# Kernel tuning notes

Measured on AMD Instinct MI355X. Metric: run time of the kernel, lower is better.

The kernel has to match this reference:

```python
import jax, jax.numpy as jnp
import numpy as np

H, L, N = 512, 4096, 64

def make_dplr_hippo(n):
    # HiPPO-LegS -> NPLR -> DPLR diagonalization (numpy, init-time only)
    p0 = np.sqrt(1 + 2 * np.arange(n))
    A = p0[:, None] * p0[None, :]
    A = -(np.tril(A) - np.diag(np.arange(n)))
    p = np.sqrt(np.arange(n) + 0.5)
    b = np.sqrt(2 * np.arange(n) + 1.0)
    S = A + p[:, None] * p[None, :]
    Lambda_re = np.full(n, np.diagonal(S).mean())
    Lambda_im, V = np.linalg.eigh(S * -1j)
    Pc = V.conj().T @ p
    Bc = V.conj().T @ b
    return Lambda_re, Lambda_im, Pc, Bc

def setup_inputs() -> dict:
    key = jax.random.key(0)
    k_u, k_c, k_s = jax.random.split(key, 3)
    lr, li, Pc, Bc = make_dplr_hippo(N)
    tile = lambda v: jnp.tile(jnp.asarray(v, jnp.float32)[None, :], (H, 1))
    dt_min, dt_max = 0.001, 0.1
    log_step = (jax.random.uniform(k_s, (H, 1), jnp.float32)
                * (np.log(dt_max) - np.log(dt_min)) + np.log(dt_min))
    return {
        "u": jax.random.normal(k_u, (H, L), jnp.float32),
        "Lambda_re": tile(lr), "Lambda_im": tile(li),
        "P_re": tile(Pc.real), "P_im": tile(Pc.imag),
        "B_re": tile(Bc.real), "B_im": tile(Bc.imag),
        "C": jax.random.normal(k_c, (H, N, 2), jnp.float32) * (0.5 ** 0.5),
        "D": jnp.ones((H, 1), jnp.float32),
        "log_step": log_step,
    }

def reference(u, Lambda_re, Lambda_im, P_re, P_im, B_re, B_im, C, D, log_step):
    # u: [H, L]; all params leading dim H (vmapped channels)
    Lam = jnp.minimum(Lambda_re, -1e-4) + 1j * Lambda_im      # [H, N]
    P = P_re + 1j * P_im                                       # [H, N]
    B = B_re + 1j * B_im                                       # [H, N]
    Cc = C[..., 0] + 1j * C[..., 1]                             # [H, N]
    step = jnp.exp(log_step)                                    # [H, 1]
    Lseq = u.shape[-1]
    Omega = jnp.exp(-2j * jnp.pi * (jnp.arange(Lseq) / Lseq)).astype(jnp.complex64)  # [L]
    g = (2.0 / step) * ((1.0 - Omega) / (1.0 + Omega))[None, :]  # [H, L]
    c = 2.0 / (1.0 + Omega)                                      # [L]
    denom = 1.0 / (g[:, :, None] - Lam[:, None, :])              # [H, L, N]
    cauchy = lambda v: jnp.einsum('hn,hln->hl', v, denom)
    k00 = cauchy(Cc.conj() * B)
    k01 = cauchy(Cc.conj() * P)
    k10 = cauchy(P.conj() * B)
    k11 = cauchy(P.conj() * P)
    atRoots = c[None, :] * (k00 - k01 * (1.0 / (1.0 + k11)) * k10)
    K = jnp.fft.ifft(atRoots, Lseq, axis=-1).real                # [H, L] conv kernel
    # causal convolution via zero-padded FFT (length 2L)
    ud = jnp.fft.rfft(u, n=2 * Lseq, axis=-1)
    Kd = jnp.fft.rfft(K, n=2 * Lseq, axis=-1)
    y = jnp.fft.irfft(ud * Kd, n=2 * Lseq, axis=-1)[..., :Lseq]
    return y + D * u
```

## Files before the change

kernel.cpp:

```cpp
#include <hip/hip_runtime.h>
#include <math.h>

#define NT 512

typedef float v2 __attribute__((ext_vector_type(2)));

__device__ __forceinline__ v2 vrot(v2 a){ return (v2){-a.y, a.x}; }
__device__ __forceinline__ v2 vconj(v2 a){ return (v2){a.x, -a.y}; }

__device__ __forceinline__ v2 pk_addrot(v2 a, v2 b){
    v2 d;
    asm("v_pk_add_f32 %0, %1, %2 op_sel:[0,1] op_sel_hi:[1,0] neg_lo:[0,1] neg_hi:[0,0]"
        : "=v"(d) : "v"(a), "v"(b));
    return d;
}
__device__ __forceinline__ v2 pk_subrot(v2 a, v2 b){
    v2 d;
    asm("v_pk_add_f32 %0, %1, %2 op_sel:[0,1] op_sel_hi:[1,0] neg_lo:[0,0] neg_hi:[0,1]"
        : "=v"(d) : "v"(a), "v"(b));
    return d;
}
__device__ __forceinline__ v2 vcmul(v2 a, v2 b){
    v2 d;
    asm("v_pk_mul_f32 %0, %1, %2 op_sel:[0,0] op_sel_hi:[0,1]"
        : "=v"(d) : "v"(a), "v"(b));
    asm("v_pk_fma_f32 %0, %1, %2, %0 op_sel:[1,1,0] op_sel_hi:[1,0,1] neg_lo:[0,1,0] neg_hi:[0,0,0]"
        : "+v"(d) : "v"(a), "v"(b));
    return d;
}
__device__ __forceinline__ v2 vcmulc(v2 a, v2 b){
    v2 d;
    asm("v_pk_mul_f32 %0, %1, %2 op_sel:[0,0] op_sel_hi:[0,1] neg_lo:[0,0] neg_hi:[0,1]"
        : "=v"(d) : "v"(a), "v"(b));
    asm("v_pk_fma_f32 %0, %1, %2, %0 op_sel:[1,1,0] op_sel_hi:[1,0,1]"
        : "+v"(d) : "v"(a), "v"(b));
    return d;
}
__device__ __forceinline__ void cacc(v2& acc, v2 w, v2 p){
    asm("v_pk_fma_f32 %0, %1, %2, %0 op_sel:[0,0,0] op_sel_hi:[1,0,1]"
        : "+v"(acc) : "s"(w), "v"(p));
    asm("v_pk_fma_f32 %0, %1, %2, %0 op_sel:[1,1,0] op_sel_hi:[0,1,1] neg_hi:[0,1,0]"
        : "+v"(acc) : "s"(w), "v"(p));
}
__device__ __forceinline__ void racc(v2& acc, v2 wp, v2 p){
    asm("v_pk_fma_f32 %0, %1, %2, %0 op_sel:[0,0,0] op_sel_hi:[1,1,1] neg_hi:[0,1,0]"
        : "+v"(acc) : "s"(wp), "v"(p));
}

__device__ __forceinline__ int SW(int e){ return e ^ (((e>>5) ^ (e>>9)) & 15); }

__device__ __forceinline__ v2& q512(v2* buf, int tbs, int k){
    return *(v2*)((char*)buf + ((tbs ^ (k<<3)) + (k<<12)));
}
__device__ __forceinline__ v2& q512u(v2* buf, int tbs, int k){
    return *(v2*)((char*)buf + (((tbs ^ 64) ^ (k<<3)) + (k<<12) + 32768));
}

__device__ __forceinline__ int d8r4(int x){
    return ((x&7)<<9) | (((x>>3)&7)<<6) | (((x>>6)&7)<<3) | ((x>>9)&7);
}
__device__ __forceinline__ int rev3(int t){
    return ((t&7)<<6) | (t&56) | ((t>>6)&7);
}

__device__ __forceinline__ void load_row(const v2* twd, int rowIdx, v2 W[7]) {
    const float4* rp4 = (const float4*)(twd + rowIdx*8);
    float4 q0 = rp4[0], q1 = rp4[1], q2 = rp4[2], q3 = rp4[3];
    W[0]=(v2){q0.x,q0.y}; W[1]=(v2){q0.z,q0.w}; W[2]=(v2){q1.x,q1.y};
    W[3]=(v2){q1.z,q1.w}; W[4]=(v2){q2.x,q2.y}; W[5]=(v2){q2.z,q2.w};
    W[6]=(v2){q3.x,q3.y};
}

__device__ __forceinline__ void dft8_inv(v2 t[8], v2 y[8]) {
    const float RH = 0.70710678f;
    v2 p  = t[0]+t[4], m  = t[0]-t[4], q  = t[2]+t[6], r  = t[2]-t[6];
    v2 E0 = p+q, E2 = p-q;
    v2 E1 = pk_addrot(m, r), E3 = pk_subrot(m, r);
    v2 p2 = t[1]+t[5], m2 = t[1]-t[5], q2 = t[3]+t[7], r2 = t[3]-t[7];
    v2 O0 = p2+q2, O2 = p2-q2;
    v2 O1 = pk_addrot(m2, r2), O3 = pk_subrot(m2, r2);
    v2 W1O = RH * pk_addrot(O1, O1);
    v2 A3  = RH * pk_addrot(O3, O3);
    y[0] = E0 + O0;  y[4] = E0 - O0;
    y[1] = E1 + W1O; y[5] = E1 - W1O;
    y[2] = pk_addrot(E2, O2); y[6] = pk_subrot(E2, O2);
    y[3] = pk_addrot(E3, A3); y[7] = pk_subrot(E3, A3);
}

__device__ __forceinline__ void dft8_inv_lo4(v2 t[8], v2 y[4]) {
    const float RH = 0.70710678f;
    v2 p  = t[0]+t[4], m  = t[0]-t[4], q  = t[2]+t[6], r  = t[2]-t[6];
    v2 E0 = p+q, E2 = p-q;
    v2 E1 = pk_addrot(m, r), E3 = pk_subrot(m, r);
    v2 p2 = t[1]+t[5], m2 = t[1]-t[5], q2 = t[3]+t[7], r2 = t[3]-t[7];
    v2 O0 = p2+q2, O2 = p2-q2;
    v2 O1 = pk_addrot(m2, r2), O3 = pk_subrot(m2, r2);
    v2 W1O = RH * pk_addrot(O1, O1);
    v2 A3  = RH * pk_addrot(O3, O3);
    y[0] = E0 + O0;
    y[1] = E1 + W1O;
    y[2] = pk_addrot(E2, O2);
    y[3] = pk_addrot(E3, A3);
}

__device__ __forceinline__ void dft8_fwd(v2 t[8], v2 y[8]) {
    const float RH = 0.70710678f;
    v2 p  = t[0]+t[4], m  = t[0]-t[4], q  = t[2]+t[6], r  = t[2]-t[6];
    v2 E0 = p+q, E2 = p-q;
    v2 E1 = pk_subrot(m, r), E3 = pk_addrot(m, r);
    v2 p2 = t[1]+t[5], m2 = t[1]-t[5], q2 = t[3]+t[7], r2 = t[3]-t[7];
    v2 O0 = p2+q2, O2 = p2-q2;
    v2 O1 = pk_subrot(m2, r2), O3 = pk_addrot(m2, r2);
    v2 W1O = RH * pk_subrot(O1, O1);
    v2 A3f = RH * pk_addrot(O3, O3);
    y[0] = E0 + O0;  y[4] = E0 - O0;
    y[1] = E1 + W1O; y[5] = E1 - W1O;
    y[2] = pk_subrot(E2, O2); y[6] = pk_addrot(E2, O2);
    y[3] = E3 - A3f; y[7] = E3 + A3f;
}


template<int Q, bool BAR>
__device__ __forceinline__ void r8_dit_inv(v2* buf, int tid, const v2* twd) {
    int j = tid & (Q-1);
    v2 W[7];
    load_row(twd, (512/Q)*j, W);
    int base = 8*tid - 7*j;
    v2 t[8];
    #pragma unroll
    for (int k = 0; k < 8; ++k) t[k] = buf[SW(base + k*Q)];
    #pragma unroll
    for (int k = 0; k < 7; ++k) t[k+1] = vcmul(t[k+1], W[k]);
    v2 y[8];
    dft8_inv(t, y);
    #pragma unroll
    for (int m = 0; m < 8; ++m) buf[SW(base + m*Q)] = y[m];
    if (BAR) __syncthreads();
    else     __builtin_amdgcn_wave_barrier();
}

template<int Q, bool BAR>
__device__ __forceinline__ void r8_dif_fwd(v2* buf, int tid, const v2* twd) {
    if (Q == 1) {
        const int b0  = tid << 6;
        const int bt  = tid << 3;
        const int mLs = (((bt>>5) ^ (bt>>9)) & 15) << 3;
        const int msU = (mLs ^ 64) + 32768;
        #pragma unroll 1
        for (int hh = 0; hh < 2; ++hh) {
            const int ms = hh ? msU : mLs;
            v2 t[8];
            #pragma unroll
            for (int k = 0; k < 8; ++k)
                t[k] = *(v2*)((char*)buf + ((b0 + (k<<3)) ^ ms));
            v2 y[8];
            dft8_fwd(t, y);
            #pragma unroll
            for (int m = 0; m < 8; ++m)
                *(v2*)((char*)buf + ((b0 + (m<<3)) ^ ms)) = y[m];
        }
        if (BAR) __syncthreads();
        else     __builtin_amdgcn_wave_barrier();
        return;
    }
    int j = tid & (Q-1);
    int baseL = 8*tid - 7*j;
    v2 W[7];
    load_row(twd, (512/Q)*j, W);
    #pragma unroll 1
    for (int hh = 0; hh < 2; ++hh) {
        int base = baseL + (hh << 12);
        v2 t[8];
        #pragma unroll
        for (int k = 0; k < 8; ++k) t[k] = buf[SW(base + k*Q)];
        v2 y[8];
        dft8_fwd(t, y);
        #pragma unroll
        for (int k = 0; k < 7; ++k) y[k+1] = vcmulc(y[k+1], W[k]);
        #pragma unroll
        for (int m = 0; m < 8; ++m) buf[SW(base + m*Q)] = y[m];
    }
    if (BAR) __syncthreads();
    else     __builtin_amdgcn_wave_barrier();
}

__global__ void __launch_bounds__(64)
s4_prep(const float* __restrict__ Lre, const float* __restrict__ Lim,
        const float* __restrict__ Pre, const float* __restrict__ Pim,
        const float* __restrict__ Bre, const float* __restrict__ Bim,
        const float* __restrict__ Cin,
        float* __restrict__ ws8, float* __restrict__ ws1,
        v2* __restrict__ twd)
{
    int b = blockIdx.x;
    if (b == (int)gridDim.x - 1) {
        const float fm = 6.2831853072f / 4096.0f;
        #pragma unroll
        for (int r = 0; r < 8; ++r) {
            int j = r*64 + (int)threadIdx.x;
            #pragma unroll
            for (int k = 0; k < 7; ++k) {
                float s, c; __sincosf(fm * (float)(j*(k+1)), &s, &c);
                twd[j*8 + k] = (v2){c, s};
            }
            twd[j*8 + 7] = (v2){1.0f, 0.0f};
        }
        return;
    }
    int idx = b*64 + threadIdx.x;
    float lre = fminf(Lre[idx], -1e-4f);
    float lim = Lim[idx];
    float pr = Pre[idx], pi = Pim[idx];
    float br = Bre[idx], bi = Bim[idx];
    float cr = Cin[2*idx], ci = Cin[2*idx+1];
    v2 cc = (v2){cr, -ci};
    v2 w00 = vcmul(cc, (v2){br, bi});
    v2 w01 = vcmul(cc, (v2){pr, pi});
    v2 w10 = vcmul((v2){pr,-pi}, (v2){br, bi});
    float* o = ws8 + idx*8;
    o[0] = -lre;  o[1] = -lim;
    o[2] = w00.x; o[3] = w00.y;
    o[4] = w01.x; o[5] = w01.y;
    o[6] = w10.x; o[7] = w10.y;
    ws1[idx] = pr*pr + pi*pi;
}

__global__ __attribute__((amdgpu_waves_per_eu(4, 4))) void __launch_bounds__(NT)
s4_fused(const float* __restrict__ u,
         const float* __restrict__ Din, const float* __restrict__ logstep,
         const float* __restrict__ ws8, const float* __restrict__ ws1,
         const v2* __restrict__ twd,
         float* __restrict__ out)
{
    __shared__ v2 buf[8192];
    const int tid = threadIdx.x;
    const int h = blockIdx.x;
    const int tbs = (tid ^ ((tid>>5) & 15)) << 3;

    const float step = expf(logstep[h]);
    const float tos  = 2.0f / step;
    const float hstep = 0.5f * step;
    const float* pp = ws8 + (h*64)*8;
    const float* pw = ws1 + h*64;
    const float4* pp4 = (const float4*)pp;

    v2 a4[4];
    #pragma unroll 1
    for (int hp = 0; hp < 2; ++hp) {
        float tv[4];
        v2 cf[4], k00[4], k01[4], k10[4], k11[4];
        const int lbase = hp*(4*NT);
        #pragma unroll
        for (int i = 0; i < 4; ++i) {
            int l = lbase + i*NT + tid;
            float ang = -6.2831855f * ((float)l * (1.0f/4096.0f));
            float sh, ch; __sincosf(0.5f*ang, &sh, &ch);
            float traw = -tos * sh * __builtin_amdgcn_rcpf(ch);
            float t = fminf(fmaxf(traw, -1e18f), 1e18f);
            tv[i] = t;
            cf[i] = (v2){1.0f, t*hstep};
            k00[i]=(v2)(0.0f); k01[i]=(v2)(0.0f); k10[i]=(v2)(0.0f); k11[i]=(v2)(0.0f);
        }
        #pragma unroll 4
        for (int n = 0; n < 64; ++n) {
            float4 A = pp4[2*n], B = pp4[2*n+1];
            float nlre = A.x, nlim = A.y;
            v2 w00 = (v2){A.z, A.w};
            v2 w01 = (v2){B.x, B.y};
            v2 w10 = (v2){B.z, B.w};
            float w11r = pw[n];
            v2 w11p = (v2){w11r, w11r};
            float lre2 = nlre*nlre;
            #pragma unroll
            for (int i = 0; i < 4; ++i) {
                float s = tv[i] + nlim;
                float inv = __builtin_amdgcn_rcpf(__builtin_fmaf(s, s, lre2));
                v2 p; p.x = nlre * inv; p.y = s * inv;
                cacc(k00[i], w00, p);
                cacc(k01[i], w01, p);
                cacc(k10[i], w10, p);
                racc(k11[i], w11p, p);
            }
        }
        #pragma unroll
        for (int i = 0; i < 4; ++i) {
            v2 opk = (v2){1.0f + k11[i].x, k11[i].y};
            float iv = __builtin_amdgcn_rcpf(opk.x*opk.x + opk.y*opk.y);
            v2 r11 = vconj(opk) * iv;
            v2 t  = vcmul(vcmul(k01[i], r11), k10[i]);
            v2 res = vcmul(cf[i], k00[i] - t);
            if (hp == 0) q512(buf, tbs, i) = res;
            else         a4[i] = res;
        }
    }
    {
        v2 t[8];
        #pragma unroll
        for (int k = 0; k < 4; ++k) t[k] = q512(buf, tbs, k);
        #pragma unroll
        for (int k = 0; k < 4; ++k) t[4+k] = a4[k];
        __syncthreads();
        v2 y[8];
        dft8_inv(t, y);
        const int tb8 = 8*rev3(tid);
        const int b8  = tb8 << 3;
        const int m8s = (((tb8>>5) ^ (tb8>>9)) & 15) << 3;
        #pragma unroll
        for (int m = 0; m < 8; ++m)
            *(v2*)((char*)buf + ((b8 + (m<<3)) ^ m8s)) = y[m];
    }
    __syncthreads();

    r8_dit_inv<8,  false>(buf, tid, twd);
    r8_dit_inv<64, true >(buf, tid, twd);

    {
        v2 W[7];
        load_row(twd, tid, W);
        v2 t[8];
        #pragma unroll
        for (int k = 0; k < 8; ++k) t[k] = q512(buf, tbs, k);
        #pragma unroll
        for (int k = 0; k < 7; ++k) t[k+1] = vcmul(t[k+1], W[k]);
        v2 y[8];
        dft8_inv(t, y);
        float uval[8];
        const float* up = u + h*4096;
        #pragma unroll
        for (int m = 0; m < 8; ++m) uval[m] = up[tid + 512*m];
        float s2, c2; __sincosf(-6.2831853072f/8192.0f*(float)tid, &s2, &c2);
        v2 cur0 = (v2){c2, s2};
        const v2 C16n = (v2){0.92387953f, -0.38268343f};
        v2 zL[8], zU[8];
        {
            v2 cur = cur0;
            #pragma unroll
            for (int k = 0; k < 8; ++k) {
                zL[k] = (v2){uval[k], y[k].x * (1.0f/4096.0f)};
                zU[k] = vcmul(zL[k], cur);
                cur = vcmul(cur, C16n);
            }
        }
        v2 s[8];
        dft8_fwd(zL, s);
        #pragma unroll
        for (int m = 1; m < 8; ++m) s[m] = vcmulc(s[m], W[m-1]);
        #pragma unroll
        for (int m = 0; m < 8; ++m) q512(buf, tbs, m) = s[m];
        dft8_fwd(zU, s);
        #pragma unroll
        for (int m = 1; m < 8; ++m) s[m] = vcmulc(s[m], W[m-1]);
        #pragma unroll
        for (int m = 0; m < 8; ++m) q512u(buf, tbs, m) = s[m];
    }
    __syncthreads();

    r8_dif_fwd<64, false>(buf, tid, twd);
    r8_dif_fwd<8,  false>(buf, tid, twd);
    r8_dif_fwd<1,  true >(buf, tid, twd);

    {
        float sb, cb; __sincosf(6.2831853072f/8192.0f*(float)tid, &sb, &cb);
        v2 cur = (v2){cb, sb};
        const v2 C16p = (v2){0.92387953f, 0.38268343f};
        v2 v[8];
        #pragma unroll 1
        for (int i = 0; i < 8; ++i) {
            int r  = i*NT + tid;
            int par = (r&1)<<12;
            int e1 = par + d8r4(r>>1);
            int e3 = e1 + 4;
            int k2c = 4096 - r;
            int e4 = ((k2c&1)<<12) + d8r4((k2c>>1)&4095);
            int e2 = (r == 0) ? 0 : (e4 + 4);
            v2 za = buf[SW(e1)];
            v2 zb = buf[SW(e2)];
            v2 zc = buf[SW(e3)];
            v2 zd = buf[SW(e4)];
            v2 U1 = 0.5f*(za + vconj(zb));
            v2 K1 = -0.5f*vrot(za - vconj(zb));
            v2 Yr = vcmul(U1, K1);
            v2 U2 = 0.5f*(zc + vconj(zd));
            v2 K2 = -0.5f*vrot(zc - vconj(zd));
            v2 Ys = vcmul(U2, K2);
            v[i] = pk_addrot(Yr + Ys, vcmul(cur, Yr - Ys));
            cur = vcmul(cur, C16p);
        }
        __syncthreads();
        v2 y[8];
        dft8_inv(v, y);
        const int tb8 = 8*rev3(tid);
        const int b8  = tb8 << 3;
        const int m8s = (((tb8>>5) ^ (tb8>>9)) & 15) << 3;
        #pragma unroll
        for (int m = 0; m < 8; ++m)
            *(v2*)((char*)buf + ((b8 + (m<<3)) ^ m8s)) = y[m];
    }
    __syncthreads();

    r8_dit_inv<8,  false>(buf, tid, twd);
    r8_dit_inv<64, true >(buf, tid, twd);

    {
        v2 W[7];
        load_row(twd, tid, W);
        v2 t[8];
        #pragma unroll
        for (int k = 0; k < 8; ++k) t[k] = q512(buf, tbs, k);
        #pragma unroll
        for (int k = 0; k < 7; ++k) t[k+1] = vcmul(t[k+1], W[k]);
        v2 y[4];
        dft8_inv_lo4(t, y);
        const float Dh = Din[h];
        const float sc = 1.0f / 8192.0f;
        const v2* u2 = (const v2*)(u + h*4096);
        v2*     out2 = (v2*)(out + h*4096);
        #pragma unroll
        for (int m = 0; m < 4; ++m) {
            int n = tid + 512*m;
            out2[n] = sc*y[m] + Dh*u2[n];
        }
    }
}

extern "C" void kernel_launch(void* const* d_in, const int* in_sizes, int n_in,
                              void* d_out, int out_size, void* d_ws, size_t ws_size,
                              hipStream_t stream)
{
    const float* u       = (const float*)d_in[0];
    const float* Lre     = (const float*)d_in[1];
    const float* Lim     = (const float*)d_in[2];
    const float* Pre     = (const float*)d_in[3];
    const float* Pim     = (const float*)d_in[4];
    const float* Bre     = (const float*)d_in[5];
    const float* Bim     = (const float*)d_in[6];
    const float* Cin     = (const float*)d_in[7];
    const float* Din     = (const float*)d_in[8];
    const float* logstep = (const float*)d_in[9];
    float* out = (float*)d_out;
    const int H = in_sizes[8];

    float* ws8 = (float*)d_ws;
    float* ws1 = ws8 + (size_t)H*64*8;
    v2*    twd = (v2*)(ws1 + (size_t)H*64);

    hipLaunchKernelGGL(s4_prep, dim3(H + 1), dim3(64), 0, stream,
                       Lre, Lim, Pre, Pim, Bre, Bim, Cin, ws8, ws1, twd);
    hipLaunchKernelGGL(s4_fused, dim3(H), dim3(NT), 0, stream,
                       u, Din, logstep, ws8, ws1, twd, out);
}
```

Before: 147.5 us.

## Repack Cauchy accumulation into SoA packed-FMA form with shared reciprocal

Restructures the inner Cauchy-kernel loop so that pairs of sequence positions share packed registers, with separate real and imaginary accumulators updated by single packed FMAs. Two denominators are reciprocated with one rcp by multiplying them and recovering each inverse through a cross-multiplication, so the transcendental count per pair is halved. The prep kernel now also stores lre^2 alongside |P|^2, and the clamp on t is tightened to 1e12 so the product of two denominators stays within float range. This adds more multiplies and more accumulator registers, and the product trick could lose precision or overflow for extreme values.

```diff
diff --git a/kernel.cpp b/kernel.cpp
--- a/kernel.cpp
+++ b/kernel.cpp
@@ -36,15 +36,60 @@
         : "+v"(d) : "v"(a), "v"(b));
     return d;
 }
-__device__ __forceinline__ void cacc(v2& acc, v2 w, v2 p){
-    asm("v_pk_fma_f32 %0, %1, %2, %0 op_sel:[0,0,0] op_sel_hi:[1,0,1]"
+
+__device__ __forceinline__ v2 pk_add_bh(v2 a, v2 s){
+    v2 d;
+    asm("v_pk_add_f32 %0, %1, %2 op_sel:[0,1] op_sel_hi:[1,1]"
+        : "=v"(d) : "v"(a), "s"(s));
+    return d;
+}
+__device__ __forceinline__ v2 pk_fma_sq_bh(v2 a, v2 s){
+    v2 d;
+    asm("v_pk_fma_f32 %0, %1, %1, %2 op_sel:[0,0,1] op_sel_hi:[1,1,1]"
+        : "=v"(d) : "v"(a), "s"(s));
+    return d;
+}
+__device__ __forceinline__ v2 pk_mul_cross(v2 a){
+    v2 d;
+    asm("v_pk_mul_f32 %0, %1, %1 op_sel:[1,0] op_sel_hi:[0,1]"
+        : "=v"(d) : "v"(a));
+    return d;
+}
+__device__ __forceinline__ v2 pk_inv_lo(v2 rr, v2 dd){
+    v2 d;
+    asm("v_pk_mul_f32 %0, %1, %2 op_sel:[0,1] op_sel_hi:[0,0]"
+        : "=v"(d) : "v"(rr), "v"(dd));
+    return d;
+}
+__device__ __forceinline__ v2 pk_inv_hi(v2 rr, v2 dd){
+    v2 d;
+    asm("v_pk_mul_f32 %0, %1, %2 op_sel:[1,1] op_sel_hi:[1,0]"
+        : "=v"(d) : "v"(rr), "v"(dd));
+    return d;
+}
+__device__ __forceinline__ v2 pk_mul_bl(v2 a, v2 s){
+    v2 d;
+    asm("v_pk_mul_f32 %0, %1, %2 op_sel:[0,0] op_sel_hi:[1,0]"
+        : "=v"(d) : "v"(a), "s"(s));
+    return d;
+}
+__device__ __forceinline__ v2 pk_mulp(v2 a, v2 b){
+    v2 d;
+    asm("v_pk_mul_f32 %0, %1, %2 op_sel:[0,0] op_sel_hi:[1,1]"
+        : "=v"(d) : "v"(a), "v"(b));
+    return d;
+}
+__device__ __forceinline__ void fmaBlo(v2& acc, v2 w, v2 p){
+    asm("v_pk_fma_f32 %0, %1, %2, %0 op_sel:[0,0,0] op_sel_hi:[0,1,1]"
         : "+v"(acc) : "s"(w), "v"(p));
-    asm("v_pk_fma_f32 %0, %1, %2, %0 op_sel:[1,1,0] op_sel_hi:[0,1,1] neg_hi:[0,1,0]"
+}
+__device__ __forceinline__ void fmaBhi(v2& acc, v2 w, v2 p){
+    asm("v_pk_fma_f32 %0, %1, %2, %0 op_sel:[1,0,0] op_sel_hi:[1,1,1]"
         : "+v"(acc) : "s"(w), "v"(p));
 }
-__device__ __forceinline__ void racc(v2& acc, v2 wp, v2 p){
-    asm("v_pk_fma_f32 %0, %1, %2, %0 op_sel:[0,0,0] op_sel_hi:[1,1,1] neg_hi:[0,1,0]"
-        : "+v"(acc) : "s"(wp), "v"(p));
+__device__ __forceinline__ void fmaBlon(v2& acc, v2 w, v2 p){
+    asm("v_pk_fma_f32 %0, %1, %2, %0 op_sel:[0,0,0] op_sel_hi:[0,1,1] neg_lo:[1,0,0] neg_hi:[1,0,0]"
+        : "+v"(acc) : "s"(w), "v"(p));
 }
 
 __device__ __forceinline__ int SW(int e){ return e ^ (((e>>5) ^ (e>>9)) & 15); }
@@ -222,7 +267,8 @@
     o[2] = w00.x; o[3] = w00.y;
     o[4] = w01.x; o[5] = w01.y;
     o[6] = w10.x; o[7] = w10.y;
-    ws1[idx] = pr*pr + pi*pi;
+    ws1[2*idx]   = pr*pr + pi*pi;
+    ws1[2*idx+1] = lre*lre;
 }
 
 __global__ __attribute__((amdgpu_waves_per_eu(4, 4))) void __launch_bounds__(NT)
@@ -241,54 +287,79 @@
     const float tos  = 2.0f / step;
     const float hstep = 0.5f * step;
     const float* pp = ws8 + (h*64)*8;
-    const float* pw = ws1 + h*64;
     const float4* pp4 = (const float4*)pp;
+    const v2* pw2 = (const v2*)(ws1 + h*128);
 
     v2 a4[4];
     #pragma unroll 1
     for (int hp = 0; hp < 2; ++hp) {
-        float tv[4];
-        v2 cf[4], k00[4], k01[4], k10[4], k11[4];
-        const int lbase = hp*(4*NT);
-        #pragma unroll
-        for (int i = 0; i < 4; ++i) {
-            int l = lbase + i*NT + tid;
-            float ang = -6.2831855f * ((float)l * (1.0f/4096.0f));
-            float sh, ch; __sincosf(0.5f*ang, &sh, &ch);
-            float traw = -tos * sh * __builtin_amdgcn_rcpf(ch);
-            float t = fminf(fmaxf(traw, -1e18f), 1e18f);
-            tv[i] = t;
-            cf[i] = (v2){1.0f, t*hstep};
-            k00[i]=(v2)(0.0f); k01[i]=(v2)(0.0f); k10[i]=(v2)(0.0f); k11[i]=(v2)(0.0f);
-        }
-        #pragma unroll 4
-        for (int n = 0; n < 64; ++n) {
-            float4 A = pp4[2*n], B = pp4[2*n+1];
-            float nlre = A.x, nlim = A.y;
-            v2 w00 = (v2){A.z, A.w};
-            v2 w01 = (v2){B.x, B.y};
-            v2 w10 = (v2){B.z, B.w};
-            float w11r = pw[n];
-            v2 w11p = (v2){w11r, w11r};
-            float lre2 = nlre*nlre;
+        v2 tvA, tvB;
+        {
+            float tv[4];
             #pragma unroll
             for (int i = 0; i < 4; ++i) {
-                float s = tv[i] + nlim;
-                float inv = __builtin_amdgcn_rcpf(__builtin_fmaf(s, s, lre2));
-                v2 p; p.x = nlre * inv; p.y = s * inv;
-                cacc(k00[i], w00, p);
-                cacc(k01[i], w01, p);
-                cacc(k10[i], w10, p);
-                racc(k11[i], w11p, p);
+                int l = hp*(4*NT) + i*NT + tid;
+                float ang = -6.2831855f * ((float)l * (1.0f/4096.0f));
+                float sh, ch; __sincosf(0.5f*ang, &sh, &ch);
+                float traw = -tos * sh * __builtin_amdgcn_rcpf(ch);
+                tv[i] = fminf(fmaxf(traw, -1e12f), 1e12f);
             }
-        }
+            tvA = (v2){tv[0], tv[1]};
+            tvB = (v2){tv[2], tv[3]};
+        }
+        v2 aX00A=(v2)(0.f), aY00A=(v2)(0.f), aX00B=(v2)(0.f), aY00B=(v2)(0.f);
+        v2 aX01A=(v2)(0.f), aY01A=(v2)(0.f), aX01B=(v2)(0.f), aY01B=(v2)(0.f);
+        v2 aX10A=(v2)(0.f), aY10A=(v2)(0.f), aX10B=(v2)(0.f), aY10B=(v2)(0.f);
+        v2 aX11A=(v2)(0.f), aY11A=(v2)(0.f), aX11B=(v2)(0.f), aY11B=(v2)(0.f);
+        #pragma unroll 2
+        for (int n = 0; n < 64; ++n) {
+            float4 A = pp4[2*n], Bq = pp4[2*n+1];
+            v2 lam = (v2){A.x, A.y};
+            v2 w00 = (v2){A.z, A.w};
+            v2 w01 = (v2){Bq.x, Bq.y};
+            v2 w10 = (v2){Bq.z, Bq.w};
+            v2 Wv  = pw2[n];
+            v2 sA = pk_add_bh(tvA, lam), sB = pk_add_bh(tvB, lam);
+            v2 dA = pk_fma_sq_bh(sA, Wv), dB = pk_fma_sq_bh(sB, Wv);
+            v2 PA = pk_mul_cross(dA), PB = pk_mul_cross(dB);
+            v2 RR;
+            RR.x = __builtin_amdgcn_rcpf(PA.x);
+            RR.y = __builtin_amdgcn_rcpf(PB.x);
+            v2 invA = pk_inv_lo(RR, dA), invB = pk_inv_hi(RR, dB);
+            v2 pxA = pk_mul_bl(invA, lam), pxB = pk_mul_bl(invB, lam);
+            v2 pyA = pk_mulp(invA, sA),    pyB = pk_mulp(invB, sB);
+            fmaBlo(aX00A, w00, pxA); fmaBhi(aX00A, w00, pyA);
+            fmaBhi(aY00A, w00, pxA); fmaBlon(aY00A, w00, pyA);
+            fmaBlo(aX00B, w00, pxB); fmaBhi(aX00B, w00, pyB);
+            fmaBhi(aY00B, w00, pxB); fmaBlon(aY00B, w00, pyB);
+            fmaBlo(aX01A, w01, pxA); fmaBhi(aX01A, w01, pyA);
+            fmaBhi(aY01A, w01, pxA); fmaBlon(aY01A, w01, pyA);
+            fmaBlo(aX01B, w01, pxB); fmaBhi(aX01B, w01, pyB);
+            fmaBhi(aY01B, w01, pxB); fmaBlon(aY01B, w01, pyB);
+            fmaBlo(aX10A, w10, pxA); fmaBhi(aX10A, w10, pyA);
+            fmaBhi(aY10A, w10, pxA); fmaBlon(aY10A, w10, pyA);
+            fmaBlo(aX10B, w10, pxB); fmaBhi(aX10B, w10, pyB);
+            fmaBhi(aY10B, w10, pxB); fmaBlon(aY10B, w10, pyB);
+            fmaBlo(aX11A, Wv, pxA);  fmaBlon(aY11A, Wv, pyA);
+            fmaBlo(aX11B, Wv, pxB);  fmaBlon(aY11B, Wv, pyB);
+        }
+        float tvv[4] = { tvA.x, tvA.y, tvB.x, tvB.y };
+        v2 k00[4] = { {aX00A.x,aY00A.x}, {aX00A.y,aY00A.y},
+                      {aX00B.x,aY00B.x}, {aX00B.y,aY00B.y} };
+        v2 k01[4] = { {aX01A.x,aY01A.x}, {aX01A.y,aY01A.y},
+                      {aX01B.x,aY01B.x}, {aX01B.y,aY01B.y} };
+        v2 k10[4] = { {aX10A.x,aY10A.x}, {aX10A.y,aY10A.y},
+                      {aX10B.x,aY10B.x}, {aX10B.y,aY10B.y} };
+        v2 k11[4] = { {aX11A.x,aY11A.x}, {aX11A.y,aY11A.y},
+                      {aX11B.x,aY11B.x}, {aX11B.y,aY11B.y} };
         #pragma unroll
         for (int i = 0; i < 4; ++i) {
             v2 opk = (v2){1.0f + k11[i].x, k11[i].y};
             float iv = __builtin_amdgcn_rcpf(opk.x*opk.x + opk.y*opk.y);
             v2 r11 = vconj(opk) * iv;
             v2 t  = vcmul(vcmul(k01[i], r11), k10[i]);
-            v2 res = vcmul(cf[i], k00[i] - t);
+            v2 cf = (v2){1.0f, tvv[i]*hstep};
+            v2 res = vcmul(cf, k00[i] - t);
             if (hp == 0) q512(buf, tbs, i) = res;
             else         a4[i] = res;
         }
@@ -442,7 +513,7 @@
 
     float* ws8 = (float*)d_ws;
     float* ws1 = ws8 + (size_t)H*64*8;
-    v2*    twd = (v2*)(ws1 + (size_t)H*64);
+    v2*    twd = (v2*)(ws1 + (size_t)H*128);
 
     hipLaunchKernelGGL(s4_prep, dim3(H + 1), dim3(64), 0, stream,
                        Lre, Lim, Pre, Pim, Bre, Bim, Cin, ws8, ws1, twd);
```

New measurement: 144.3 us. 2.2% less time.
